# Kernel optimization log

Measured on AMD Instinct MI355X. Metric: run time of the kernel, lower is better.

## Reference

```python
import jax, jax.numpy as jnp
import numpy as np


@jax.custom_vjp
def quantize(x):
    # sign with straight-through estimator (TL_Sign_QuantizeGrad: clipped identity)
    return jnp.sign(x)


def _quantize_fwd(x):
    return jnp.sign(x), x


def _quantize_bwd(x, g):
    # pass gradient through where |x| <= 1
    return (g * (jnp.abs(x) <= 1.0).astype(g.dtype),)


quantize.defvjp(_quantize_fwd, _quantize_bwd)


def setup_inputs() -> dict:
    key = jax.random.key(0)
    k1, k2 = jax.random.split(key)
    x = jax.random.normal(k1, (32, 112, 112, 128), dtype=jnp.float32)
    W = jax.random.normal(k2, (3, 3, 128, 256), dtype=jnp.float32) * 0.02
    b = jnp.zeros((256,), dtype=jnp.float32)
    return {"x": x, "W": W, "b": b}


def reference(x, W, b):
    # binarize weights to {-1, +1}; bias stays full precision; act = identity
    Wq = quantize(W)
    out = jax.lax.conv_general_dilated(
        x, Wq,
        window_strides=(1, 1),
        padding="SAME",
        dimension_numbers=("NHWC", "HWIO", "NHWC"),
    )
    return out + b
```

## Files before the change

### kernel.cpp

```cpp
#include <hip/hip_runtime.h>
#include <hip/hip_bf16.h>

typedef __attribute__((ext_vector_type(8))) short short8;
typedef __attribute__((ext_vector_type(8))) __bf16 bf16x8;
typedef __attribute__((ext_vector_type(4))) float f32x4;
typedef __attribute__((ext_vector_type(4))) unsigned int uint4v;

#define HW      112
#define CIN     128
#define COUT    256
#define IMG_PIX (112*112)
#define NPIX    (32*112*112)
#define MTILES  (NPIX/128)
#define NTILES  (COUT/128)
#define NBLK    (MTILES*NTILES)

__device__ __forceinline__ unsigned short f2bf(float f) {
    unsigned int u = __float_as_uint(f);
    u = (u + 0x7FFFu + ((u >> 16) & 1u)) >> 16;
    return (unsigned short)u;
}

__global__ __launch_bounds__(256) void quantW_kernel(const float* __restrict__ W,
                                                     unsigned short* __restrict__ Wq) {
    int idx = blockIdx.x * 256 + threadIdx.x;
    if (idx >= 9 * CIN * COUT) return;
    int co   = idx & 255;
    int rest = idx >> 8;
    int ci   = rest & 127;
    int tap  = rest >> 7;
    float w = W[idx];
    unsigned short s = (w > 0.f) ? 0x3F80u : ((w < 0.f) ? 0xBF80u : 0u);
    Wq[(tap * COUT + co) * CIN + ci] = s;
}

__global__ __launch_bounds__(256, 2) void bconv_mfma(const float* __restrict__ x,
                                                     const unsigned short* __restrict__ Wq,
                                                     const float* __restrict__ bias,
                                                     float* __restrict__ out) {
    __shared__ __align__(16) unsigned short ldsA[128 * 128];
    __shared__ __align__(16) unsigned short ldsB[128 * 128];

    const int tid  = threadIdx.x;
    const int lane = tid & 63;
    const int wave = tid >> 6;
    const int wr   = wave >> 1;
    const int wc   = wave & 1;

    int bid = blockIdx.x;
    int swz = (bid & 7) * (NBLK / 8) + (bid >> 3);
    const int mt = swz >> 1;
    const int nt = swz & 1;
    const int m0 = mt * 128;
    const int n0 = nt * 128;

    const int sg    = tid & 15;
    const int srow0 = tid >> 4;

    int hh[8], ww[8], pbase[8];
#pragma unroll
    for (int i = 0; i < 8; ++i) {
        int row = srow0 + i * 16;
        int p   = m0 + row;
        int rem = p % IMG_PIX;
        hh[i]   = rem / HW;
        ww[i]   = rem % HW;
        pbase[i] = p * CIN;
    }

    f32x4 acc[4][4];
#pragma unroll
    for (int mi = 0; mi < 4; ++mi)
#pragma unroll
        for (int ni = 0; ni < 4; ++ni)
            acc[mi][ni] = (f32x4)(0.f);

    for (int tap = 0; tap < 9; ++tap) {
        const int dh   = tap / 3 - 1;
        const int dw   = tap - (tap / 3) * 3 - 1;
        const int doff = (dh * HW + dw) * CIN;

        __syncthreads();

#pragma unroll
        for (int i = 0; i < 8; ++i) {
            int row = srow0 + i * 16;
            bool valid = ((unsigned)(hh[i] + dh) < HW) & ((unsigned)(ww[i] + dw) < HW);
            float f0, f1, f2, f3, f4, f5, f6, f7;
            if (valid) {
                const float* src = x + pbase[i] + doff + sg * 8;
                float4 v0 = *(const float4*)(src);
                float4 v1 = *(const float4*)(src + 4);
                f0 = v0.x; f1 = v0.y; f2 = v0.z; f3 = v0.w;
                f4 = v1.x; f5 = v1.y; f6 = v1.z; f7 = v1.w;
            } else {
                f0 = f1 = f2 = f3 = f4 = f5 = f6 = f7 = 0.f;
            }
            unsigned int w0 = (unsigned int)f2bf(f0) | ((unsigned int)f2bf(f1) << 16);
            unsigned int w1 = (unsigned int)f2bf(f2) | ((unsigned int)f2bf(f3) << 16);
            unsigned int w2 = (unsigned int)f2bf(f4) | ((unsigned int)f2bf(f5) << 16);
            unsigned int w3 = (unsigned int)f2bf(f6) | ((unsigned int)f2bf(f7) << 16);
            uint4v v; v.x = w0; v.y = w1; v.z = w2; v.w = w3;
            int byteoff = row * 256 + ((sg * 16) ^ ((row & 7) << 4));
            *(uint4v*)((char*)ldsA + byteoff) = v;
        }

#pragma unroll
        for (int i = 0; i < 8; ++i) {
            int row = srow0 + i * 16;
            const unsigned short* src = Wq + (tap * COUT + n0 + row) * CIN + sg * 8;
            uint4v v = *(const uint4v*)src;
            int byteoff = row * 256 + ((sg * 16) ^ ((row & 7) << 4));
            *(uint4v*)((char*)ldsB + byteoff) = v;
        }

        __syncthreads();

#pragma unroll
        for (int ks = 0; ks < 4; ++ks) {
            const int kb = ks * 64 + ((lane >> 4) * 16);
            short8 af[4], bfv[4];
#pragma unroll
            for (int mi = 0; mi < 4; ++mi) {
                int row = wr * 64 + mi * 16 + (lane & 15);
                int off = row * 256 + (kb ^ ((row & 7) << 4));
                af[mi] = *(const short8*)((const char*)ldsA + off);
            }
#pragma unroll
            for (int ni = 0; ni < 4; ++ni) {
                int row = wc * 64 + ni * 16 + (lane & 15);
                int off = row * 256 + (kb ^ ((row & 7) << 4));
                bfv[ni] = *(const short8*)((const char*)ldsB + off);
            }
#pragma unroll
            for (int mi = 0; mi < 4; ++mi)
#pragma unroll
                for (int ni = 0; ni < 4; ++ni)
                    acc[mi][ni] = __builtin_amdgcn_mfma_f32_16x16x32_bf16(
                        __builtin_bit_cast(bf16x8, af[mi]),
                        __builtin_bit_cast(bf16x8, bfv[ni]),
                        acc[mi][ni], 0, 0, 0);
        }
    }

    const int crow = (lane >> 4) * 4;
    const int ccol = lane & 15;
#pragma unroll
    for (int ni = 0; ni < 4; ++ni) {
        int co = n0 + wc * 64 + ni * 16 + ccol;
        float bv = bias[co];
#pragma unroll
        for (int mi = 0; mi < 4; ++mi) {
            int prow = m0 + wr * 64 + mi * 16 + crow;
#pragma unroll
            for (int r = 0; r < 4; ++r) {
                out[(size_t)(prow + r) * COUT + co] = acc[mi][ni][r] + bv;
            }
        }
    }
}

extern "C" void kernel_launch(void* const* d_in, const int* in_sizes, int n_in,
                              void* d_out, int out_size, void* d_ws, size_t ws_size,
                              hipStream_t stream) {
    const float* x = (const float*)d_in[0];
    const float* W = (const float*)d_in[1];
    const float* b = (const float*)d_in[2];
    float* out = (float*)d_out;
    unsigned short* Wq = (unsigned short*)d_ws;

    hipLaunchKernelGGL(quantW_kernel, dim3((9 * CIN * COUT + 255) / 256), dim3(256), 0, stream, W, Wq);
    hipLaunchKernelGGL(bconv_mfma, dim3(NBLK), dim3(256), 0, stream, x, Wq, b, out);
}
```

Baseline: 909.5 us.

## Pre-pad and convert input to bf16, use async double-buffered 256x256 conv tiles

Adds a pre-pass that writes a zero-padded bf16 copy of the input, so the conv loop needs no bounds checks and reads half the bytes. A new conv kernel uses 512-thread blocks with 256x256 tiles covering all output channels, and loads into LDS directly via global_load_lds. The K loop is split into 18 double-buffered stages with manual vmcnt waits, plus s_setprio around the MFMA block. The cost is an extra pass writing and reading the padded tensor, a dependence on a large workspace, and 128 accumulator registers per thread, which limits occupancy.

```diff
diff --git a/kernel.cpp b/kernel.cpp
--- a/kernel.cpp
+++ b/kernel.cpp
@@ -11,14 +11,51 @@
 #define COUT    256
 #define IMG_PIX (112*112)
 #define NPIX    (32*112*112)
+#define PAD     114
+#define PAD_PIX (114*114)
+#define XP_PIXELS (32*PAD_PIX)
+#define XP_BYTES ((size_t)XP_PIXELS*CIN*2)
+#define WQ_BYTES ((size_t)9*COUT*CIN*2)
 #define MTILES  (NPIX/128)
 #define NTILES  (COUT/128)
 #define NBLK    (MTILES*NTILES)
+#define NBLK2   (NPIX/256)
 
 __device__ __forceinline__ unsigned short f2bf(float f) {
     unsigned int u = __float_as_uint(f);
     u = (u + 0x7FFFu + ((u >> 16) & 1u)) >> 16;
     return (unsigned short)u;
+}
+
+__device__ __forceinline__ void gload16(const void* g, void* l) {
+    __builtin_amdgcn_global_load_lds(
+        (const __attribute__((address_space(1))) unsigned int*)g,
+        (__attribute__((address_space(3))) unsigned int*)l, 16, 0, 0);
+}
+
+__global__ __launch_bounds__(256) void pad_cvt(const float* __restrict__ x,
+                                               unsigned short* __restrict__ xp) {
+    int idx = blockIdx.x * 256 + threadIdx.x;
+    if (idx >= XP_PIXELS * 16) return;
+    int p  = idx >> 4;
+    int c8 = idx & 15;
+    int n   = p / PAD_PIX;
+    int rem = p - n * PAD_PIX;
+    int hp  = rem / PAD;
+    int wp  = rem - hp * PAD;
+    short8 v;
+    if ((unsigned)(hp - 1) < HW && (unsigned)(wp - 1) < HW) {
+        const float* src = x + (size_t)((n * HW + hp - 1) * HW + wp - 1) * CIN + c8 * 8;
+        float4 a = *(const float4*)src;
+        float4 b = *(const float4*)(src + 4);
+        v[0] = (short)f2bf(a.x); v[1] = (short)f2bf(a.y);
+        v[2] = (short)f2bf(a.z); v[3] = (short)f2bf(a.w);
+        v[4] = (short)f2bf(b.x); v[5] = (short)f2bf(b.y);
+        v[6] = (short)f2bf(b.z); v[7] = (short)f2bf(b.w);
+    } else {
+        v[0]=v[1]=v[2]=v[3]=v[4]=v[5]=v[6]=v[7] = 0;
+    }
+    *(short8*)(xp + (size_t)p * CIN + c8 * 8) = v;
 }
 
 __global__ __launch_bounds__(256) void quantW_kernel(const float* __restrict__ W,
@@ -32,6 +69,118 @@
     float w = W[idx];
     unsigned short s = (w > 0.f) ? 0x3F80u : ((w < 0.f) ? 0xBF80u : 0u);
     Wq[(tap * COUT + co) * CIN + ci] = s;
+}
+
+__global__ __launch_bounds__(512, 2) void bconv_big(const unsigned short* __restrict__ xp,
+                                                    const unsigned short* __restrict__ Wq,
+                                                    const float* __restrict__ bias,
+                                                    float* __restrict__ out) {
+    __shared__ __align__(16) unsigned short lds[65536];
+
+    const int tid  = threadIdx.x;
+    const int lane = tid & 63;
+    const int w    = tid >> 6;
+    const int wr   = w >> 2;
+    const int wc   = w & 3;
+    const int l15  = lane & 15;
+    const int l7   = lane & 7;
+    const int q    = lane >> 4;
+
+    int bid = blockIdx.x;
+    int swz = (bid & 7) * (NBLK2 / 8) + (bid >> 3);
+    const int m0 = swz * 256;
+
+    const int cig = (lane & 7) ^ ((lane >> 3) & 7);
+    int srcA_off[4];
+    int srcB_off[4];
+    const int rbase = w * 32 + (lane >> 3);
+#pragma unroll
+    for (int i = 0; i < 4; ++i) {
+        int r = rbase + i * 8;
+        int p = m0 + r;
+        int n   = p / IMG_PIX;
+        int rem = p - n * IMG_PIX;
+        int h   = rem / HW;
+        int ww2 = rem - h * HW;
+        int pad_pix = (n * PAD + h + 1) * PAD + (ww2 + 1);
+        srcA_off[i] = pad_pix * 256 + cig * 16;
+        srcB_off[i] = r * 256 + cig * 16;
+    }
+
+    const char* xpB = (const char*)xp;
+    const char* wqB = (const char*)Wq;
+
+    f32x4 acc[8][4];
+#pragma unroll
+    for (int mi = 0; mi < 8; ++mi)
+#pragma unroll
+        for (int ni = 0; ni < 4; ++ni)
+            acc[mi][ni] = (f32x4)(0.f);
+
+    auto issue = [&](int t, int bsel) {
+        int tap  = t >> 1;
+        int ci0b = (t & 1) * 128;
+        int d3   = tap / 3;
+        int aoff = ((d3 - 1) * PAD + (tap - d3 * 3 - 1)) * 256 + ci0b;
+        const char* wsl = wqB + tap * 65536 + ci0b;
+        unsigned short* Ad = &lds[bsel * 16384 + (w * 32) * 64];
+        unsigned short* Bd = &lds[32768 + bsel * 16384 + (w * 32) * 64];
+#pragma unroll
+        for (int i = 0; i < 4; ++i) {
+            gload16(xpB + srcA_off[i] + aoff, Ad + i * 512);
+            gload16(wsl + srcB_off[i],        Bd + i * 512);
+        }
+    };
+
+    issue(0, 0);
+    issue(1, 1);
+
+    for (int t = 0; t < 18; ++t) {
+        if (t < 17) asm volatile("s_waitcnt vmcnt(8)" ::: "memory");
+        else        asm volatile("s_waitcnt vmcnt(0)" ::: "memory");
+        asm volatile("s_barrier" ::: "memory");
+
+        const unsigned short* A = &lds[(t & 1) * 16384];
+        const unsigned short* B = &lds[32768 + (t & 1) * 16384];
+
+#pragma unroll
+        for (int ks = 0; ks < 2; ++ks) {
+            const int ch = (((ks * 4 + q) ^ l7) * 8);
+            short8 bfrag[4], afrag[8];
+#pragma unroll
+            for (int ni = 0; ni < 4; ++ni)
+                bfrag[ni] = *(const short8*)&B[(wc * 64 + ni * 16 + l15) * 64 + ch];
+#pragma unroll
+            for (int mi = 0; mi < 8; ++mi)
+                afrag[mi] = *(const short8*)&A[(wr * 128 + mi * 16 + l15) * 64 + ch];
+            __builtin_amdgcn_s_setprio(1);
+#pragma unroll
+            for (int mi = 0; mi < 8; ++mi)
+#pragma unroll
+                for (int ni = 0; ni < 4; ++ni)
+                    acc[mi][ni] = __builtin_amdgcn_mfma_f32_16x16x32_bf16(
+                        __builtin_bit_cast(bf16x8, afrag[mi]),
+                        __builtin_bit_cast(bf16x8, bfrag[ni]),
+                        acc[mi][ni], 0, 0, 0);
+            __builtin_amdgcn_s_setprio(0);
+        }
+
+        asm volatile("s_barrier" ::: "memory");
+        if (t + 2 < 18) issue(t + 2, t & 1);
+    }
+
+#pragma unroll
+    for (int ni = 0; ni < 4; ++ni) {
+        int co = wc * 64 + ni * 16 + l15;
+        float bv = bias[co];
+#pragma unroll
+        for (int mi = 0; mi < 8; ++mi) {
+            int prow = m0 + wr * 128 + mi * 16 + q * 4;
+#pragma unroll
+            for (int r = 0; r < 4; ++r)
+                out[(size_t)(prow + r) * COUT + co] = acc[mi][ni][r] + bv;
+        }
+    }
 }
 
 __global__ __launch_bounds__(256, 2) void bconv_mfma(const float* __restrict__ x,
@@ -167,8 +316,16 @@
     const float* W = (const float*)d_in[1];
     const float* b = (const float*)d_in[2];
     float* out = (float*)d_out;
-    unsigned short* Wq = (unsigned short*)d_ws;
-
-    hipLaunchKernelGGL(quantW_kernel, dim3((9 * CIN * COUT + 255) / 256), dim3(256), 0, stream, W, Wq);
-    hipLaunchKernelGGL(bconv_mfma, dim3(NBLK), dim3(256), 0, stream, x, Wq, b, out);
-}
+
+    if (ws_size >= XP_BYTES + WQ_BYTES) {
+        unsigned short* xp = (unsigned short*)d_ws;
+        unsigned short* Wq = (unsigned short*)((char*)d_ws + XP_BYTES);
+        hipLaunchKernelGGL(pad_cvt, dim3((XP_PIXELS * 16 + 255) / 256), dim3(256), 0, stream, x, xp);
+        hipLaunchKernelGGL(quantW_kernel, dim3((9 * CIN * COUT + 255) / 256), dim3(256), 0, stream, W, Wq);
+        hipLaunchKernelGGL(bconv_big, dim3(NBLK2), dim3(512), 0, stream, xp, Wq, b, out);
+    } else {
+        unsigned short* Wq = (unsigned short*)d_ws;
+        hipLaunchKernelGGL(quantW_kernel, dim3((9 * CIN * COUT + 255) / 256), dim3(256), 0, stream, W, Wq);
+        hipLaunchKernelGGL(bconv_mfma, dim3(NBLK), dim3(256), 0, stream, x, Wq, b, out);
+    }
+}
```

New measurement: 786.1 us. 1.16x faster.
